# Kernel tuning notes

Hardware: AMD Instinct MI355X
Metric: run time of the kernel (lower is better)

Reference implementation:

```python
import jax, jax.numpy as jnp
import numpy as np

B, T, D_IN, D_H, N_H = 8, 1024, 512, 64, 8
PAD_TAIL = 128


def setup_inputs() -> dict:
    key = jax.random.key(0)
    ks = jax.random.split(key, 7)
    keys = jax.random.normal(ks[0], (B, T, D_IN), jnp.float32)
    queries = jax.random.normal(ks[1], (B, T, D_IN), jnp.float32)
    values = jax.random.normal(ks[2], (B, T, D_IN), jnp.float32)
    # truncated_normal(stddev=0.01) in the original; plain normal*0.01 is a faithful stand-in
    Wk = jax.random.normal(ks[3], (D_IN, D_H, N_H), jnp.float32) * 0.01
    Wq = jax.random.normal(ks[4], (D_IN, D_H, N_H), jnp.float32) * 0.01
    Wv = jax.random.normal(ks[5], (D_IN, D_H, N_H), jnp.float32) * 0.01
    key_seq = jax.random.randint(ks[6], (B, T), 0, 32000)
    key_seq = key_seq.at[:, -PAD_TAIL:].set(-1)  # -1 marks padding positions
    return {"keys": keys, "queries": queries, "values": values,
            "Wk": Wk, "Wq": Wq, "Wv": Wv, "key_seq": key_seq}


def reference(keys, queries, values, Wk, Wq, Wv, key_seq):
    # projections: (b, t, i) x (i, d, h) -> (b, t, d, h)
    Kh = jnp.einsum('bti,idh->btdh', keys, Wk)
    Qh = jnp.einsum('bti,idh->btdh', queries, Wq)
    Vh = jnp.einsum('bti,idh->btdh', values, Wv)

    # scores: i indexes keys, j indexes queries -> (b, Tk, Tq, h)
    scores = jnp.einsum('bidh,bjdh->bijh', Kh, Qh)

    dt = scores.dtype
    # padding mask over key positions (key_seq == -1 -> -1000)
    pad_mask = (-1000.0 * (1.0 - jnp.sign(key_seq + 1).astype(dt)))[:, :, None, None]
    # causal mask: disallow key index i > query index j (matrix_band_part(_, 0, -1) keeps i<=j)
    Tk, Tq = Kh.shape[1], Qh.shape[1]
    caus_mask = -1000.0 * jnp.tril(jnp.ones((Tk, Tq), dt), k=-1)
    mask = pad_mask + caus_mask[None, :, :, None]

    # NB: original adds mask BEFORE scaling, so the -1000 is also scaled. Keep that order.
    hidden_size = Kh.shape[2]
    scores = (scores + mask) / (hidden_size ** 0.5)

    # softmax over the key axis (axis=1)
    attn = jax.nn.softmax(scores, axis=1)

    # aggregate values: (b, i, j, h) x (b, i, d, h) -> (b, j, d, h)
    h_t = jnp.einsum('bijh,bidh->bjdh', attn, Vh)

    # tf.concat(tf.split(h_t, H, axis=-1), axis=2)[:, :, :, 0]
    # == per-head feature blocks laid out head-major along the feature axis
    b, j, d, nh = h_t.shape
    return h_t.transpose(0, 1, 3, 2).reshape(b, j, nh * d)
```

## Files before the change

kernel.cpp:

```cpp
#include <hip/hip_runtime.h>
#include <hip/hip_bf16.h>

#define B_SZ 8
#define T_SZ 1024
#define D_IN 512
#define D_H  64
#define N_H  8

typedef __hip_bfloat16 bf16;
using short8  = __attribute__((ext_vector_type(8))) short;
using short4v = __attribute__((ext_vector_type(4))) short;
using f32x4   = __attribute__((ext_vector_type(4))) float;

__device__ __forceinline__ unsigned short f2bf(float f) {
    union { __hip_bfloat16 b; unsigned short u; } c;
    c.b = __float2bfloat16(f);
    return c.u;
}

__global__ __launch_bounds__(256) void wt_kernel(
    const float* __restrict__ Wk, const float* __restrict__ Wq,
    const float* __restrict__ Wv, unsigned short* __restrict__ Wt)
{
    const int mat = blockIdx.y;
    const float* W = (mat == 0) ? Wk : (mat == 1) ? Wq : Wv;
    int idx = blockIdx.x * 256 + threadIdx.x;
    float v = W[idx];
    int k = idx >> 9, c = idx & 511;
    int h = c & 7, d = c >> 3;
    Wt[(((size_t)mat * 8 + h) * 64 + d) * 512 + k] = f2bf(v);
}

__global__ __launch_bounds__(256) void proj_kernel(
    const float* __restrict__ keys, const float* __restrict__ queries,
    const float* __restrict__ values,
    const unsigned short* __restrict__ Wt, unsigned short* __restrict__ KQVb)
{
    const int tid = threadIdx.x;
    const int m0  = blockIdx.x * 128;
    const int mh  = blockIdx.y;
    const int mat = mh >> 3, h = mh & 7;

    const float* X = (mat == 0) ? keys : (mat == 1) ? queries : values;
    const unsigned short* WT = Wt + (size_t)mh * (64 * 512);
    unsigned short* P = KQVb + (size_t)mat * ((size_t)B_SZ * N_H * T_SZ * D_H);

    __shared__ __align__(16) unsigned short Xst[128 * 72];
    __shared__ __align__(16) unsigned short Wst[64 * 72];

    const int wid = tid >> 6, lane = tid & 63;
    const int quad = lane >> 4, l15 = lane & 15;

    f32x4 acc[2][4];
    #pragma unroll
    for (int a = 0; a < 2; ++a)
        #pragma unroll
        for (int n = 0; n < 4; ++n) acc[a][n] = (f32x4){0.f, 0.f, 0.f, 0.f};

    const float4* X4 = (const float4*)X;

    for (int kc = 0; kc < 8; ++kc) {
        const int k0 = kc * 64;
        __syncthreads();
        #pragma unroll
        for (int q2 = 0; q2 < 8; ++q2) {
            int e = tid + q2 * 256;
            int r = e >> 4, c4 = e & 15;
            float4 v = X4[(size_t)(m0 + r) * (D_IN / 4) + (k0 >> 2) + c4];
            short4v s = {(short)f2bf(v.x), (short)f2bf(v.y),
                         (short)f2bf(v.z), (short)f2bf(v.w)};
            *(short4v*)&Xst[r * 72 + c4 * 4] = s;
        }
        #pragma unroll
        for (int q2 = 0; q2 < 2; ++q2) {
            int e = tid + q2 * 256;
            int d = e >> 3, ch = e & 7;
            *(short8*)&Wst[d * 72 + ch * 8] =
                *(const short8*)&WT[(size_t)d * 512 + k0 + ch * 8];
        }
        __syncthreads();
        #pragma unroll
        for (int ic = 0; ic < 2; ++ic) {
            short8 a0 = *(const short8*)&Xst[(wid*32      + l15) * 72 + ic*32 + quad*8];
            short8 a1 = *(const short8*)&Xst[(wid*32 + 16 + l15) * 72 + ic*32 + quad*8];
            #pragma unroll
            for (int nt = 0; nt < 4; ++nt) {
                short8 bf = *(const short8*)&Wst[(nt*16 + l15) * 72 + ic*32 + quad*8];
                acc[0][nt] = __builtin_amdgcn_mfma_f32_16x16x32_bf16(a0, bf, acc[0][nt], 0, 0, 0);
                acc[1][nt] = __builtin_amdgcn_mfma_f32_16x16x32_bf16(a1, bf, acc[1][nt], 0, 0, 0);
            }
        }
    }

    #pragma unroll
    for (int mt = 0; mt < 2; ++mt)
        #pragma unroll
        for (int r = 0; r < 4; ++r) {
            int mrow = m0 + wid * 32 + mt * 16 + quad * 4 + r;
            int bb = mrow >> 10, t = mrow & 1023;
            size_t base = (((size_t)(bb * N_H + h)) * T_SZ + t) * D_H;
            #pragma unroll
            for (int nt = 0; nt < 4; ++nt)
                P[base + nt * 16 + l15] = f2bf(acc[mt][nt][r]);
        }
}

#define SCALE  0.18033688f
#define MASKV -180.33688f

__global__ __launch_bounds__(512, 4) void attn_kernel(
    const unsigned short* __restrict__ Qb, const unsigned short* __restrict__ Kb,
    const unsigned short* __restrict__ Vb,
    const int* __restrict__ key_seq, float* __restrict__ out)
{
    const int tid  = threadIdx.x;
    const int bid  = blockIdx.x;
    const int pair = bid >> 6;
    const int b    = (bid >> 3) & 7;
    const int h    = bid & 7;
    const int wid  = tid >> 6, lane = tid & 63;
    const int quad = lane >> 4, l15 = lane & 15;

    __shared__ __align__(16) unsigned short Kst[2][64 * 72];
    __shared__ __align__(16) unsigned short VTst[2][64 * 72];
    __shared__ __align__(16) float spadf[2][64];
    __shared__ int tflags[16];

    const size_t bh = (size_t)(b * N_H + h) * T_SZ;

    const int strip_j0 = (wid < 4) ? (15 - pair) * 64 : pair * 64;
    const int j0w = strip_j0 + (wid & 3) * 16;
    const int jg  = j0w + l15;
    const int ntmax = 16 - pair;

    short8 qf0 = *(const short8*)&Qb[(bh + jg) * D_H + quad * 8];
    short8 qf1 = *(const short8*)&Qb[(bh + jg) * D_H + 32 + quad * 8];

    {
        int ka  = key_seq[b * T_SZ + wid * 64 + lane];
        int kb2 = key_seq[b * T_SZ + 512 + wid * 64 + lane];
        unsigned long long ba  = __ballot(ka  != -1);
        unsigned long long bb2 = __ballot(kb2 != -1);
        if (lane == 0) {
            tflags[wid]     = (ba  != 0ull ? 1 : 0) | (ba  != ~0ull ? 2 : 0);
            tflags[8 + wid] = (bb2 != 0ull ? 1 : 0) | (bb2 != ~0ull ? 2 : 0);
        }
    }

    const int sk_row = tid >> 3, sk_c = tid & 7;
    const int sv_i = lane, sv_ch = wid;
    const int sv_col = (sv_i & 3) | ((sv_i & 16) >> 2) | ((sv_i & 4) << 1)
                     | ((sv_i & 8) << 1) | (sv_i & 32);

    short8 kreg = *(const short8*)&Kb[(bh + sk_row) * D_H + sk_c * 8];
    short8 vreg = *(const short8*)&Vb[(bh + sv_i) * D_H + sv_ch * 8];
    int ksv = (tid < 64) ? key_seq[b * T_SZ + tid] : -1;

    __syncthreads();

    unsigned tmask = 1u, pmask = 0u;
    #pragma unroll
    for (int t = 0; t < 16; ++t) {
        int f = tflags[t];
        tmask |= (unsigned)(f & 1) << t;
        pmask |= (unsigned)((f >> 1) & 1) << t;
    }
    tmask &= (unsigned)((1ull << ntmax) - 1ull);
    tmask |= 1u;

    *(short8*)&Kst[0][sk_row * 72 + sk_c * 8] = kreg;
    #pragma unroll
    for (int e = 0; e < 8; ++e)
        VTst[0][(sv_ch * 8 + e) * 72 + sv_col] = (unsigned short)vreg[e];
    if (tid < 64) spadf[0][tid] = (ksv == -1) ? MASKV : 0.f;
    __syncthreads();

    float m = -1e30f, l = 0.f;
    f32x4 o0 = {0.f,0.f,0.f,0.f}, o1 = o0, o2 = o0, o3 = o0;

    unsigned rem = tmask & ~1u;
    int tcur = 0, nb = 0;
    for (;;) {
        int tnext = -1;
        if (rem) { tnext = __ffs((int)rem) - 1; rem &= rem - 1; }
        if (tnext >= 0) {
            const size_t r0 = bh + tnext * 64;
            kreg = *(const short8*)&Kb[(r0 + sk_row) * D_H + sk_c * 8];
            vreg = *(const short8*)&Vb[(r0 + sv_i) * D_H + sv_ch * 8];
            if (tid < 64) ksv = key_seq[b * T_SZ + tnext * 64 + tid];
        }

        const int i0 = tcur * 64;
        if (i0 <= j0w + 15) {
            const bool haspad = (pmask >> tcur) & 1u;
            const bool needC  = (i0 + 63 > j0w);
            float sv[16];
            #pragma unroll
            for (int it = 0; it < 4; ++it) {
                f32x4 s = {0.f,0.f,0.f,0.f};
                short8 a0 = *(const short8*)&Kst[nb][(it*16 + l15) * 72 + quad*8];
                s = __builtin_amdgcn_mfma_f32_16x16x32_bf16(a0, qf0, s, 0, 0, 0);
                short8 a1 = *(const short8*)&Kst[nb][(it*16 + l15) * 72 + 32 + quad*8];
                s = __builtin_amdgcn_mfma_f32_16x16x32_bf16(a1, qf1, s, 0, 0, 0);
                f32x4 sp = {0.f,0.f,0.f,0.f};
                if (haspad) sp = *(const f32x4*)&spadf[nb][it*16 + quad*4];
                #pragma unroll
                for (int r = 0; r < 4; ++r) {
                    float v = __builtin_fmaf(s[r], SCALE, sp[r]);
                    if (needC && (i0 + it*16 + quad*4 + r > jg)) v += MASKV;
                    sv[it*4 + r] = v;
                }
            }

            float mt = sv[0];
            #pragma unroll
            for (int k = 1; k < 16; ++k) mt = fmaxf(mt, sv[k]);
            mt = fmaxf(mt, __shfl_xor(mt, 16));
            mt = fmaxf(mt, __shfl_xor(mt, 32));
            const float mnew  = fmaxf(m, mt);
            const float alpha = exp2f(m - mnew);
            float p[16], ls = 0.f;
            #pragma unroll
            for (int k = 0; k < 16; ++k) {
                p[k] = exp2f(sv[k] - mnew);
                ls += p[k];
            }
            ls += __shfl_xor(ls, 16);
            ls += __shfl_xor(ls, 32);
            l = l * alpha + ls;
            m = mnew;
            o0 *= alpha; o1 *= alpha; o2 *= alpha; o3 *= alpha;

            short8 pf0, pf1;
            #pragma unroll
            for (int e = 0; e < 8; ++e) {
                pf0[e] = (short)f2bf(p[e]);
                pf1[e] = (short)f2bf(p[8 + e]);
            }
            short8 a;
            a = *(const short8*)&VTst[nb][(     l15) * 72 +      quad * 8];
            o0 = __builtin_amdgcn_mfma_f32_16x16x32_bf16(a, pf0, o0, 0, 0, 0);
            a = *(const short8*)&VTst[nb][(     l15) * 72 + 32 + quad * 8];
            o0 = __builtin_amdgcn_mfma_f32_16x16x32_bf16(a, pf1, o0, 0, 0, 0);
            a = *(const short8*)&VTst[nb][(16 + l15) * 72 +      quad * 8];
            o1 = __builtin_amdgcn_mfma_f32_16x16x32_bf16(a, pf0, o1, 0, 0, 0);
            a = *(const short8*)&VTst[nb][(16 + l15) * 72 + 32 + quad * 8];
            o1 = __builtin_amdgcn_mfma_f32_16x16x32_bf16(a, pf1, o1, 0, 0, 0);
            a = *(const short8*)&VTst[nb][(32 + l15) * 72 +      quad * 8];
            o2 = __builtin_amdgcn_mfma_f32_16x16x32_bf16(a, pf0, o2, 0, 0, 0);
            a = *(const short8*)&VTst[nb][(32 + l15) * 72 + 32 + quad * 8];
            o2 = __builtin_amdgcn_mfma_f32_16x16x32_bf16(a, pf1, o2, 0, 0, 0);
            a = *(const short8*)&VTst[nb][(48 + l15) * 72 +      quad * 8];
            o3 = __builtin_amdgcn_mfma_f32_16x16x32_bf16(a, pf0, o3, 0, 0, 0);
            a = *(const short8*)&VTst[nb][(48 + l15) * 72 + 32 + quad * 8];
            o3 = __builtin_amdgcn_mfma_f32_16x16x32_bf16(a, pf1, o3, 0, 0, 0);
        }

        if (tnext < 0) break;

        const int nb2 = nb ^ 1;
        *(short8*)&Kst[nb2][sk_row * 72 + sk_c * 8] = kreg;
        #pragma unroll
        for (int e = 0; e < 8; ++e)
            VTst[nb2][(sv_ch * 8 + e) * 72 + sv_col] = (unsigned short)vreg[e];
        if (tid < 64) spadf[nb2][tid] = (ksv == -1) ? MASKV : 0.f;
        __syncthreads();
        tcur = tnext; nb = nb2;
    }

    const float inv = 1.f / l;
    float* op = out + ((size_t)b * T_SZ + jg) * (N_H * D_H) + h * D_H + quad * 4;
    *(f32x4*)(op +  0) = o0 * inv;
    *(f32x4*)(op + 16) = o1 * inv;
    *(f32x4*)(op + 32) = o2 * inv;
    *(f32x4*)(op + 48) = o3 * inv;
}

extern "C" void kernel_launch(void* const* d_in, const int* in_sizes, int n_in,
                              void* d_out, int out_size, void* d_ws, size_t ws_size,
                              hipStream_t stream) {
    const float* keys    = (const float*)d_in[0];
    const float* queries = (const float*)d_in[1];
    const float* values  = (const float*)d_in[2];
    const float* Wk      = (const float*)d_in[3];
    const float* Wq      = (const float*)d_in[4];
    const float* Wv      = (const float*)d_in[5];
    const int*   key_seq = (const int*)d_in[6];

    const size_t per = (size_t)B_SZ * N_H * T_SZ * D_H;
    unsigned short* KQVb = (unsigned short*)d_ws;
    unsigned short* Kb = KQVb;
    unsigned short* Qb = KQVb + per;
    unsigned short* Vb = KQVb + 2 * per;
    unsigned short* Wt = KQVb + 3 * per;

    wt_kernel<<<dim3(512 * 512 / 256, 3), 256, 0, stream>>>(Wk, Wq, Wv, Wt);
    proj_kernel<<<dim3((B_SZ * T_SZ) / 128, 3 * N_H), 256, 0, stream>>>(
        keys, queries, values, Wt, KQVb);
    attn_kernel<<<dim3(512), dim3(512), 0, stream>>>(
        Qb, Kb, Vb, key_seq, (float*)d_out);
}
```

Baseline: 156.8 us.

## Enlarge projection GEMM tile to 128x128 spanning two heads per block

The projection kernel now computes a 128x128 output tile (two heads' worth of columns) per block, with each wave owning a 64x64 sub-tile of 4x4 MFMA accumulators instead of 32x64. This cuts redundant re-reading and fp32->bf16 conversion of the input activations, which were reloaded once per head (24 times per row), down to 4 times per row, and raises MFMA work per LDS fragment load. In exchange it uses more accumulator registers and launches fewer blocks (768 vs 1536), with a launch bound hint of 3 blocks per CU.

```diff
diff --git a/kernel.cpp b/kernel.cpp
--- a/kernel.cpp
+++ b/kernel.cpp
@@ -31,31 +31,32 @@
     Wt[(((size_t)mat * 8 + h) * 64 + d) * 512 + k] = f2bf(v);
 }
 
-__global__ __launch_bounds__(256) void proj_kernel(
+__global__ __launch_bounds__(256, 3) void proj_kernel(
     const float* __restrict__ keys, const float* __restrict__ queries,
     const float* __restrict__ values,
     const unsigned short* __restrict__ Wt, unsigned short* __restrict__ KQVb)
 {
     const int tid = threadIdx.x;
     const int m0  = blockIdx.x * 128;
-    const int mh  = blockIdx.y;
-    const int mat = mh >> 3, h = mh & 7;
+    const int n0  = blockIdx.y * 128;
+    const int mat = blockIdx.z;
 
     const float* X = (mat == 0) ? keys : (mat == 1) ? queries : values;
-    const unsigned short* WT = Wt + (size_t)mh * (64 * 512);
+    const unsigned short* WT = Wt + (size_t)mat * (512 * 512);
     unsigned short* P = KQVb + (size_t)mat * ((size_t)B_SZ * N_H * T_SZ * D_H);
 
     __shared__ __align__(16) unsigned short Xst[128 * 72];
-    __shared__ __align__(16) unsigned short Wst[64 * 72];
+    __shared__ __align__(16) unsigned short Wst[128 * 72];
 
     const int wid = tid >> 6, lane = tid & 63;
     const int quad = lane >> 4, l15 = lane & 15;
-
-    f32x4 acc[2][4];
+    const int wr = (wid >> 1) * 64, wc = (wid & 1) * 64;
+
+    f32x4 acc[4][4];
     #pragma unroll
-    for (int a = 0; a < 2; ++a)
-        #pragma unroll
-        for (int n = 0; n < 4; ++n) acc[a][n] = (f32x4){0.f, 0.f, 0.f, 0.f};
+    for (int i = 0; i < 4; ++i)
+        #pragma unroll
+        for (int n = 0; n < 4; ++n) acc[i][n] = (f32x4){0.f, 0.f, 0.f, 0.f};
 
     const float4* X4 = (const float4*)X;
 
@@ -72,36 +73,44 @@
             *(short4v*)&Xst[r * 72 + c4 * 4] = s;
         }
         #pragma unroll
-        for (int q2 = 0; q2 < 2; ++q2) {
+        for (int q2 = 0; q2 < 4; ++q2) {
             int e = tid + q2 * 256;
-            int d = e >> 3, ch = e & 7;
-            *(short8*)&Wst[d * 72 + ch * 8] =
-                *(const short8*)&WT[(size_t)d * 512 + k0 + ch * 8];
+            int row = e >> 3, ch = e & 7;
+            *(short8*)&Wst[row * 72 + ch * 8] =
+                *(const short8*)&WT[(size_t)(n0 + row) * 512 + k0 + ch * 8];
         }
         __syncthreads();
         #pragma unroll
         for (int ic = 0; ic < 2; ++ic) {
-            short8 a0 = *(const short8*)&Xst[(wid*32      + l15) * 72 + ic*32 + quad*8];
-            short8 a1 = *(const short8*)&Xst[(wid*32 + 16 + l15) * 72 + ic*32 + quad*8];
+            short8 af[4], bf[4];
+            #pragma unroll
+            for (int mt = 0; mt < 4; ++mt)
+                af[mt] = *(const short8*)&Xst[(wr + mt*16 + l15) * 72 + ic*32 + quad*8];
+            #pragma unroll
+            for (int nt = 0; nt < 4; ++nt)
+                bf[nt] = *(const short8*)&Wst[(wc + nt*16 + l15) * 72 + ic*32 + quad*8];
+            #pragma unroll
+            for (int mt = 0; mt < 4; ++mt)
+                #pragma unroll
+                for (int nt = 0; nt < 4; ++nt)
+                    acc[mt][nt] = __builtin_amdgcn_mfma_f32_16x16x32_bf16(
+                        af[mt], bf[nt], acc[mt][nt], 0, 0, 0);
+        }
+    }
+
+    #pragma unroll
+    for (int mt = 0; mt < 4; ++mt)
+        #pragma unroll
+        for (int r = 0; r < 4; ++r) {
+            int mrow = m0 + wr + mt * 16 + quad * 4 + r;
+            int bb = mrow >> 10, t = mrow & 1023;
             #pragma unroll
             for (int nt = 0; nt < 4; ++nt) {
-                short8 bf = *(const short8*)&Wst[(nt*16 + l15) * 72 + ic*32 + quad*8];
-                acc[0][nt] = __builtin_amdgcn_mfma_f32_16x16x32_bf16(a0, bf, acc[0][nt], 0, 0, 0);
-                acc[1][nt] = __builtin_amdgcn_mfma_f32_16x16x32_bf16(a1, bf, acc[1][nt], 0, 0, 0);
+                int c = n0 + wc + nt * 16 + l15;
+                int h = c >> 6, d = c & 63;
+                P[(((size_t)(bb * N_H + h)) * T_SZ + t) * D_H + d] =
+                    f2bf(acc[mt][nt][r]);
             }
-        }
-    }
-
-    #pragma unroll
-    for (int mt = 0; mt < 2; ++mt)
-        #pragma unroll
-        for (int r = 0; r < 4; ++r) {
-            int mrow = m0 + wid * 32 + mt * 16 + quad * 4 + r;
-            int bb = mrow >> 10, t = mrow & 1023;
-            size_t base = (((size_t)(bb * N_H + h)) * T_SZ + t) * D_H;
-            #pragma unroll
-            for (int nt = 0; nt < 4; ++nt)
-                P[base + nt * 16 + l15] = f2bf(acc[mt][nt][r]);
         }
 }
 
@@ -295,7 +304,7 @@
     unsigned short* Wt = KQVb + 3 * per;
 
     wt_kernel<<<dim3(512 * 512 / 256, 3), 256, 0, stream>>>(Wk, Wq, Wv, Wt);
-    proj_kernel<<<dim3((B_SZ * T_SZ) / 128, 3 * N_H), 256, 0, stream>>>(
+    proj_kernel<<<dim3(64, 4, 3), 256, 0, stream>>>(
         keys, queries, values, Wt, KQVb);
     attn_kernel<<<dim3(512), dim3(512), 0, stream>>>(
         Qb, Kb, Vb, key_seq, (float*)d_out);
```

Result: no change. 156.5 us (-0.2%).
